# Kernel optimization log

Measured on AMD Instinct MI355X. Metric: run time of the kernel, lower is better.

The kernel has to match this reference:

```python
import jax, jax.numpy as jnp
import numpy as np
import math

N, E, D, R, L = 20000, 640000, 128, 16, 3
R_MAX = math.sqrt(2.0)
CENTERS = jnp.linspace(0.0, R_MAX, R)          # GaussianRBF centers on [0, sqrt(2)]
GAMMA = 1.0 / (2.0 * (R_MAX / (R - 1)) ** 2)   # 1/(2*sigma^2), sigma = center spacing


def _mlp(x, w1, b1, w2, b2):
    # mlp([din, d_h, dout]): Linear -> SiLU -> Linear (dropout=0.0)
    return jax.nn.silu(x @ w1 + b1) @ w2 + b2


def _ln(x, g, b):
    mu = jnp.mean(x, axis=-1, keepdims=True)
    v = jnp.var(x, axis=-1, keepdims=True)
    return (x - mu) * jax.lax.rsqrt(v + 1e-5) * g + b


def _time_emb(t):
    # SinusoidalEmbedding(dim=D)
    half = D // 2
    freqs = jnp.exp(-math.log(10000.0) * jnp.arange(half, dtype=jnp.float32) / (half - 1))
    a = t * freqs
    return jnp.concatenate([jnp.sin(a), jnp.cos(a)])


def setup_inputs():
    key = jax.random.key(0)
    ks = jax.random.split(key, 16)
    s = 0.05
    p = {}
    p["x_t"] = jax.random.normal(ks[0], (N, 3), dtype=jnp.float32)
    p["edge_index"] = jax.random.randint(ks[1], (2, E), 0, N)
    p["t"] = 25
    p["time_w1"] = jax.random.normal(ks[2], (D, D)) * s
    p["time_b1"] = jnp.zeros((D,))
    p["time_w2"] = jax.random.normal(ks[3], (D, D)) * s
    p["time_b2"] = jnp.zeros((D,))
    p["nodein_w1"] = jax.random.normal(ks[4], (3 + D, D)) * s
    p["nodein_b1"] = jnp.zeros((D,))
    p["nodein_w2"] = jax.random.normal(ks[5], (D, D)) * s
    p["nodein_b2"] = jnp.zeros((D,))
    p["phim_w1"] = jax.random.normal(ks[6], (L, 2 * D + R, D)) * s
    p["phim_b1"] = jnp.zeros((L, D))
    p["phim_w2"] = jax.random.normal(ks[7], (L, D, D)) * s
    p["phim_b2"] = jnp.zeros((L, D))
    p["phih_w1"] = jax.random.normal(ks[8], (L, 2 * D, D)) * s
    p["phih_b1"] = jnp.zeros((L, D))
    p["phih_w2"] = jax.random.normal(ks[9], (L, D, D)) * s
    p["phih_b2"] = jnp.zeros((L, D))
    p["ln_g"] = jnp.ones((L, D))
    p["ln_b"] = jnp.zeros((L, D))
    p["out_w1"] = jax.random.normal(ks[10], (D, D)) * s
    p["out_b1"] = jnp.zeros((D,))
    p["out_w2"] = jax.random.normal(ks[11], (D, 3)) * s
    p["out_b2"] = jnp.zeros((3,))
    return p


def reference(x_t, edge_index, t,
              time_w1, time_b1, time_w2, time_b2,
              nodein_w1, nodein_b1, nodein_w2, nodein_b2,
              phim_w1, phim_b1, phim_w2, phim_b2,
              phih_w1, phih_b1, phih_w2, phih_b2,
              ln_g, ln_b,
              out_w1, out_b1, out_w2, out_b2):
    # GraphDenoiser.forward: one denoiser call of the diffusion sampling loop.
    n = x_t.shape[0]
    src, dst = edge_index[0], edge_index[1]

    te = _mlp(_time_emb(jnp.asarray(t, jnp.float32)), time_w1, time_b1, time_w2, time_b2)
    h = _mlp(jnp.concatenate([x_t, jnp.broadcast_to(te, (n, D))], axis=-1),
             nodein_w1, nodein_b1, nodein_w2, nodein_b2)

    # edge geometry is fixed across layers (depends only on x_t)
    dx = x_t[src, :2] - x_t[dst, :2]                     # [E, 2]
    r = jnp.sqrt(jnp.sum(dx * dx, axis=-1) + 1e-8)       # [E]
    rbf = jnp.exp(-GAMMA * (r[:, None] - CENTERS) ** 2)  # [E, R]

    for i in range(L):  # WeightedInvariantMPNNLayer x L (edge_weight == 1)
        m_in = jnp.concatenate([h[src], h[dst], rbf], axis=-1)      # [E, 2D+R]
        m = _mlp(m_in, phim_w1[i], phim_b1[i], phim_w2[i], phim_b2[i])
        agg = jax.ops.segment_sum(m, dst, num_segments=n)           # scatter_sum
        h_up = _mlp(jnp.concatenate([h, agg], axis=-1),
                    phih_w1[i], phih_b1[i], phih_w2[i], phih_b2[i])
        h = _ln(h + h_up, ln_g[i], ln_b[i])

    return _mlp(h, out_w1, out_b1, out_w2, out_b2)  # predicted eps, [N, 3]
```

## Files before the change

kernel.cpp:

```cpp
#include <hip/hip_runtime.h>

typedef unsigned short u16;
typedef unsigned int u32;

#define NNODES 20000
#define NEDGES 640000
#define RBF_GAMMA 56.25f
#define SQRT2 1.4142135623730951f
#define PITCH 132
#define BPITCH 136

typedef __bf16 bf16x8 __attribute__((ext_vector_type(8)));
typedef __bf16 bf16x2 __attribute__((ext_vector_type(2)));
typedef float f32x4 __attribute__((ext_vector_type(4)));

__device__ __forceinline__ float b2f(u16 u) {
    union { float f; u32 i; } x; x.i = ((u32)u) << 16; return x.f;
}
__device__ __forceinline__ float hi2f(u32 w) {
    union { float f; u32 i; } x; x.i = w & 0xffff0000u; return x.f;
}
__device__ __forceinline__ float lo2f(u32 w) {
    union { float f; u32 i; } x; x.i = w << 16; return x.f;
}
__device__ __forceinline__ u16 f2b(float f) {
    union { float f; u32 i; } x; x.f = f;
    u32 r = (x.i + 0x7fffu + ((x.i >> 16) & 1u)) >> 16;
    return (u16)r;
}
__device__ __forceinline__ u32 pack2(float a, float b) {
#if __has_builtin(__builtin_amdgcn_cvt_pk_bf16_f32)
    union { bf16x2 v; u32 u; } x;
    x.v = __builtin_amdgcn_cvt_pk_bf16_f32(a, b);
    return x.u;
#else
    return (u32)f2b(a) | ((u32)f2b(b) << 16);
#endif
}
__device__ __forceinline__ float silu(float v) {
    return v * __builtin_amdgcn_rcpf(1.0f + __expf(-v));
}
__device__ __forceinline__ void fma4(float4 w, float4 s, float& acc) {
    acc = fmaf(w.x, s.x, acc);
    acc = fmaf(w.y, s.y, acc);
    acc = fmaf(w.z, s.z, acc);
    acc = fmaf(w.w, s.w, acc);
}

__global__ __launch_bounds__(256) void k_hist(const int* __restrict__ ei, int* __restrict__ hist) {
    int e = blockIdx.x * 256 + threadIdx.x;
    atomicAdd(&hist[ei[NEDGES + e]], 1);
}

__global__ __launch_bounds__(1024) void k_scan(const int* __restrict__ hist,
                                               int* __restrict__ row_ptr,
                                               int* __restrict__ cursor) {
    __shared__ int psum[1024];
    int t = threadIdx.x;
    int base = t * 20;
    int s = 0;
    if (base < NNODES)
        for (int i = 0; i < 20; ++i) s += hist[base + i];
    psum[t] = s;
    __syncthreads();
    for (int off = 1; off < 1024; off <<= 1) {
        int v = (t >= off) ? psum[t - off] : 0;
        __syncthreads();
        psum[t] += v;
        __syncthreads();
    }
    int excl = psum[t] - s;
    if (base < NNODES) {
        int run = excl;
        for (int i = 0; i < 20; ++i) {
            row_ptr[base + i] = run;
            cursor[base + i] = run;
            run += hist[base + i];
        }
    }
    if (t == 1023) row_ptr[NNODES] = psum[1023];
}

__global__ __launch_bounds__(256) void k_scatter(const int* __restrict__ ei, int* __restrict__ cursor,
                                                 int* __restrict__ ssrc, int* __restrict__ sdst) {
    int e = blockIdx.x * 256 + threadIdx.x;
    int d = ei[NEDGES + e];
    int pos = atomicAdd(&cursor[d], 1);
    ssrc[pos] = ei[e];
    sdst[pos] = d;
}

__global__ __launch_bounds__(256) void k_prep_wr(const float* __restrict__ pmw1,
                                                 const float* __restrict__ pmb1,
                                                 u16* __restrict__ Wr) {
    int id = blockIdx.x * 256 + threadIdx.x;
    if (id >= 1536) return;
    int l = id / 512; int r = id - l * 512;
    int nt = r >> 6, lane = r & 63;
    int col = nt * 16 + (lane & 15);
    alignas(16) u16 tmp[8];
    #pragma unroll
    for (int jj = 0; jj < 8; ++jj) {
        int kk = (lane >> 4) * 8 + jj;
        float v = 0.f;
        if (kk < 16) v = pmw1[l * 34816 + (256 + kk) * 128 + col];
        else if (kk == 16) v = pmb1[l * 128 + col];
        tmp[jj] = f2b(v);
    }
    *(uint4*)(Wr + (size_t)id * 8) = *(const uint4*)tmp;
}

struct BfM { const float* s[18]; };
__global__ __launch_bounds__(256) void k_prep_bf(BfM bf, u16* __restrict__ dst) {
    int id = blockIdx.x * 256 + threadIdx.x;
    if (id >= 36864) return;
    int mat = id >> 11;
    bool lomode = (mat >= 13 && mat != 16);
    int r = id & 2047;
    int kc = r >> 9;
    int r2 = r & 511;
    int nt = r2 >> 6, lane = r2 & 63;
    int col = nt * 16 + (lane & 15);
    int kb = kc * 32 + (lane >> 4) * 8;
    const float* src = bf.s[mat];
    alignas(16) u16 tmp[8];
    #pragma unroll
    for (int jj = 0; jj < 8; ++jj) {
        float v = src[(kb + jj) * 128 + col];
        u16 h = f2b(v);
        tmp[jj] = lomode ? f2b(v - b2f(h)) : h;
    }
    *(uint4*)(dst + (size_t)id * 8) = *(const uint4*)tmp;
}

__global__ __launch_bounds__(256) void k_prep_mbf(const float* __restrict__ Mp, u16* __restrict__ dst) {
    int id = blockIdx.x * 256 + threadIdx.x;
    if (id >= 12288) return;
    int mat = id >> 11;
    int l = mat >> 1, lomode = mat & 1;
    int r = id & 2047;
    int kc = r >> 9;
    int r2 = r & 511;
    int nt = r2 >> 6, lane = r2 & 63;
    int col = nt * 16 + (lane & 15);
    int kb = kc * 32 + (lane >> 4) * 8;
    const float* src = Mp + (size_t)l * 16384;
    alignas(16) u16 tmp[8];
    #pragma unroll
    for (int jj = 0; jj < 8; ++jj) {
        int k = kb + jj;
        float v = src[(k >> 2) * 512 + col * 4 + (k & 3)];
        u16 h = f2b(v);
        tmp[jj] = lomode ? f2b(v - b2f(h)) : h;
    }
    *(uint4*)(dst + (size_t)id * 8) = *(const uint4*)tmp;
}

struct PackM { const float* s[3]; float* d[3]; int K[3]; };
__global__ __launch_bounds__(256) void k_pack(PackM pm) {
    int m = blockIdx.y;
    int idx = blockIdx.x * 256 + threadIdx.x;
    if (idx >= pm.K[m] * 128) return;
    int k = idx >> 7, j = idx & 127;
    pm.d[m][(k >> 2) * 512 + j * 4 + (k & 3)] = pm.s[m][idx];
}

__global__ __launch_bounds__(256) void k_prep_m(const float* __restrict__ pmw2,
        const float* __restrict__ pmb2, const float* __restrict__ V1p,
        float* __restrict__ Mp, float* __restrict__ bvv) {
    const int l = blockIdx.y, bx = blockIdx.x;
    const float* V1 = V1p + (size_t)l * 32768;
    const int tid = threadIdx.x;
    const int w = tid >> 6, lane = tid & 63;
    const int cg = lane & 15, ng = lane >> 4;
    const int jc0 = w * 32 + cg * 2, jc1 = jc0 + 1;
    __shared__ alignas(16) float W2L[16][PITCH];
    __shared__ float b2L[128];
    if (bx < 8) {
        const float4* src = (const float4*)(pmw2 + (size_t)l * 16384 + bx * 16 * 128);
        for (int q = tid; q < 512; q += 256) {
            int row = q >> 5, part = q & 31;
            *(float4*)&W2L[row][part * 4] = src[q];
        }
        __syncthreads();
        int r0 = ng * 4;
        float acc[4][2];
        #pragma unroll
        for (int n = 0; n < 4; ++n) { acc[n][0] = 0.f; acc[n][1] = 0.f; }
        for (int mm = 0; mm < 32; ++mm) {
            float4 wa = *(const float4*)(V1 + (32 + mm) * 512 + jc0 * 4);
            float4 wb = *(const float4*)(V1 + (32 + mm) * 512 + jc1 * 4);
            #pragma unroll
            for (int n = 0; n < 4; ++n) {
                float4 s4 = *(const float4*)&W2L[r0 + n][mm * 4];
                fma4(wa, s4, acc[n][0]);
                fma4(wb, s4, acc[n][1]);
            }
        }
        #pragma unroll
        for (int n = 0; n < 4; ++n) {
            int kg = bx * 16 + r0 + n;
            Mp[(size_t)l * 16384 + (kg >> 2) * 512 + jc0 * 4 + (kg & 3)] = acc[n][0];
            Mp[(size_t)l * 16384 + (kg >> 2) * 512 + jc1 * 4 + (kg & 3)] = acc[n][1];
        }
    } else {
        if (tid < 128) b2L[tid] = pmb2[l * 128 + tid];
        __syncthreads();
        if (ng == 0) {
            float a0 = 0.f, a1 = 0.f;
            for (int mm = 0; mm < 32; ++mm) {
                float4 wa = *(const float4*)(V1 + (32 + mm) * 512 + jc0 * 4);
                float4 wb = *(const float4*)(V1 + (32 + mm) * 512 + jc1 * 4);
                float4 s4 = *(const float4*)&b2L[mm * 4];
                fma4(wa, s4, a0);
                fma4(wb, s4, a1);
            }
            bvv[l * 128 + jc0] = a0;
            bvv[l * 128 + jc1] = a1;
        }
    }
}

__global__ __launch_bounds__(128) void k_time(const int* __restrict__ tptr,
        const float* __restrict__ tw1, const float* __restrict__ tb1,
        const float* __restrict__ tw2, const float* __restrict__ tb2,
        const float* __restrict__ nw1, const float* __restrict__ nb1,
        float* __restrict__ base1) {
    __shared__ float emb[128], hid[128], te[128];
    int j = threadIdx.x;
    int raw = tptr[0];
    float tv;
    if (raw >= 0 && raw < (1 << 24)) tv = (float)raw;
    else tv = __int_as_float(raw);
    float fr = expf(-9.210340371976184f * (float)(j & 63) / 63.0f);
    float a = tv * fr;
    emb[j] = (j < 64) ? sinf(a) : cosf(a);
    __syncthreads();
    float acc = tb1[j];
    for (int k = 0; k < 128; ++k) acc += emb[k] * tw1[k * 128 + j];
    hid[j] = silu(acc);
    __syncthreads();
    acc = tb2[j];
    for (int k = 0; k < 128; ++k) acc += hid[k] * tw2[k * 128 + j];
    te[j] = acc;
    __syncthreads();
    acc = nb1[j];
    for (int k = 0; k < 128; ++k) acc += te[k] * nw1[(3 + k) * 128 + j];
    base1[j] = acc;
}

__global__ __launch_bounds__(256) void k_h0(const float* __restrict__ x, const float* __restrict__ base1,
        const float* __restrict__ nw1, const u16* __restrict__ nw2h, const u16* __restrict__ nw2l,
        const float* __restrict__ nb2, const u16* __restrict__ Yw,
        float* __restrict__ hf, u16* __restrict__ Ysrc, u16* __restrict__ Ydst) {
    const int tid = threadIdx.x;
    const int w = tid >> 6, lane = tid & 63;
    const int cg = lane & 15, ng = lane >> 4;
    const int jc0 = w * 32 + cg * 2, jc1 = jc0 + 1;
    const int n0 = ng * 4;
    const int base = blockIdx.x * 16;
    const int lrow = lane & 15, quad = lane >> 4;
    __shared__ alignas(16) float xl[16][4];
    __shared__ alignas(16) u16 hih[16 * BPITCH], hil[16 * BPITCH];
    __shared__ alignas(16) u16 hb16[16 * BPITCH];
    if (tid < 48) { int n = tid / 3, cc = tid - n * 3; xl[n][cc] = x[(size_t)(base + n) * 3 + cc]; }
    __syncthreads();
    {
        float w0a = nw1[jc0], w0b = nw1[jc1];
        float w1a = nw1[128 + jc0], w1b = nw1[128 + jc1];
        float w2a = nw1[256 + jc0], w2b = nw1[256 + jc1];
        float ba = base1[jc0], bb = base1[jc1];
        #pragma unroll
        for (int n = 0; n < 4; ++n) {
            int row = n0 + n;
            float x0 = xl[row][0], x1 = xl[row][1], x2 = xl[row][2];
            float va = silu(ba + x0 * w0a + x1 * w1a + x2 * w2a);
            float vb = silu(bb + x0 * w0b + x1 * w1b + x2 * w2b);
            u32 hw = pack2(va, vb);
            *(u32*)&hih[row * BPITCH + jc0] = hw;
            *(u32*)&hil[row * BPITCH + jc0] = pack2(va - lo2f(hw), vb - hi2f(hw));
        }
    }
    __syncthreads();
    {
        bf16x8 ah[4], al[4];
        #pragma unroll
        for (int kc = 0; kc < 4; ++kc) {
            ah[kc] = *(const bf16x8*)(hih + lrow * BPITCH + kc * 32 + quad * 8);
            al[kc] = *(const bf16x8*)(hil + lrow * BPITCH + kc * 32 + quad * 8);
        }
        #pragma unroll
        for (int t = 0; t < 2; ++t) {
            int nt = w * 2 + t;
            f32x4 a4 = {0.f, 0.f, 0.f, 0.f};
            #pragma unroll
            for (int kc = 0; kc < 4; ++kc) {
                size_t o = (size_t)((kc * 8 + nt) * 512 + lane * 8);
                bf16x8 bh = *(const bf16x8*)(nw2h + o);
                bf16x8 bl = *(const bf16x8*)(nw2l + o);
                a4 = __builtin_amdgcn_mfma_f32_16x16x32_bf16(ah[kc], bh, a4, 0, 0, 0);
                a4 = __builtin_amdgcn_mfma_f32_16x16x32_bf16(al[kc], bh, a4, 0, 0, 0);
                a4 = __builtin_amdgcn_mfma_f32_16x16x32_bf16(ah[kc], bl, a4, 0, 0, 0);
            }
            int colC = nt * 16 + lrow;
            float bC = nb2[colC];
            #pragma unroll
            for (int r = 0; r < 4; ++r) {
                int R = quad * 4 + r;
                float v = a4[r] + bC;
                hf[(size_t)(base + R) * 128 + colC] = v;
                hb16[R * BPITCH + colC] = f2b(v);
            }
        }
    }
    __syncthreads();
    {
        const int mat = w >> 1, half = w & 1;
        bf16x8 a[4];
        #pragma unroll
        for (int kc = 0; kc < 4; ++kc)
            a[kc] = *(const bf16x8*)(hb16 + lrow * BPITCH + kc * 32 + quad * 8);
        u16* dst = mat ? Ydst : Ysrc;
        #pragma unroll
        for (int t = 0; t < 4; ++t) {
            int nt = half * 4 + t;
            f32x4 a4 = {0.f, 0.f, 0.f, 0.f};
            #pragma unroll
            for (int kc = 0; kc < 4; ++kc) {
                bf16x8 b = *(const bf16x8*)(Yw + (size_t)(((mat * 4 + kc) * 8 + nt) * 512 + lane * 8));
                a4 = __builtin_amdgcn_mfma_f32_16x16x32_bf16(a[kc], b, a4, 0, 0, 0);
            }
            #pragma unroll
            for (int r = 0; r < 4; ++r)
                dst[(size_t)(base + quad * 4 + r) * 128 + nt * 16 + lrow] = f2b(a4[r]);
        }
    }
}

__global__ __launch_bounds__(512, 8) void k_edge(
        const u16* __restrict__ Ysrc, const u16* __restrict__ Ydst,
        const float* __restrict__ x,
        const int* __restrict__ ssrc, const int* __restrict__ sdst,
        const u16* __restrict__ Wr,
        float* __restrict__ s_glob) {
    __shared__ alignas(16) u16 sst[128 * 72];
    __shared__ alignas(16) u16 ys[64 * 128];
    __shared__ float rv[64];
    __shared__ int s_d[65];
    __shared__ int s_s[64];
    const int tid = threadIdx.x;
    const int e0 = blockIdx.x * 64;
    if (tid < 64) {
        int s = ssrc[e0 + tid], d = sdst[e0 + tid];
        s_s[tid] = s; s_d[tid] = d;
        float ddx = x[s * 3] - x[d * 3];
        float ddy = x[s * 3 + 1] - x[d * 3 + 1];
        rv[tid] = sqrtf(ddx * ddx + ddy * ddy + 1e-8f);
    } else if (tid == 64) {
        s_d[64] = -1;
    }
    __syncthreads();
    #pragma unroll
    for (int i = 0; i < 2; ++i) {
        int cch = tid + i * 512;
        int e = cch >> 4, part = cch & 15;
        *(uint4*)(ys + e * 128 + part * 8) = *(const uint4*)(Ysrc + (size_t)s_s[e] * 128 + part * 8);
    }
    const int w = tid >> 6, lane = tid & 63;
    const int m = w & 3, nh = w >> 2;
    const int lrow = lane & 15, quad = lane >> 4;
    float r = rv[m * 16 + lrow];
    union { bf16x8 v; u16 u[8]; } af;
    #pragma unroll
    for (int j = 0; j < 8; ++j) {
        int kk = quad * 8 + j;
        float v;
        if (kk < 16) {
            float dd = r - SQRT2 * (float)kk / 15.0f;
            v = __expf(-RBF_GAMMA * dd * dd);
        } else v = (kk == 16) ? 1.0f : 0.0f;
        af.u[j] = f2b(v);
    }
    {
        const u16* Bp = Wr + lane * 8;
        #pragma unroll
        for (int t = 0; t < 4; ++t) {
            int nt = nh * 4 + t;
            f32x4 a4 = {0.f, 0.f, 0.f, 0.f};
            bf16x8 b = *(const bf16x8*)(Bp + nt * 512);
            a4 = __builtin_amdgcn_mfma_f32_16x16x32_bf16(af.v, b, a4, 0, 0, 0);
            int col = nt * 16 + lrow;
            u32 lo = pack2(a4[0], a4[1]);
            u32 hi = pack2(a4[2], a4[3]);
            *(uint2*)(sst + col * 72 + m * 16 + quad * 4) = make_uint2(lo, hi);
        }
    }
    __syncthreads();
    {
        const int col = tid & 127, q = tid >> 7;
        const int r0 = q * 16;
        float a = 0.f;
        int cd = s_d[r0];
        float yd = b2f(Ydst[(size_t)cd * 128 + col]);
        #pragma unroll
        for (int h = 0; h < 2; ++h) {
            uint4 c0 = *(const uint4*)(sst + col * 72 + r0 + h * 8);
            float sv8[8];
            sv8[0] = lo2f(c0.x); sv8[1] = hi2f(c0.x);
            sv8[2] = lo2f(c0.y); sv8[3] = hi2f(c0.y);
            sv8[4] = lo2f(c0.z); sv8[5] = hi2f(c0.z);
            sv8[6] = lo2f(c0.w); sv8[7] = hi2f(c0.w);
            #pragma unroll
            for (int i = 0; i < 8; ++i) {
                int rr = r0 + h * 8 + i;
                int nd = s_d[rr + 1];
                float v = sv8[i] + b2f(ys[rr * 128 + col]) + yd;
                a += silu(v);
                bool last = (h == 1 && i == 7);
                if (last || nd != cd) {
                    atomicAdd(&s_glob[(size_t)cd * 128 + col], a);
                    a = 0.f;
                    if (!last && nd != cd)
                        yd = b2f(Ydst[(size_t)nd * 128 + col]);
                }
                cd = nd;
            }
        }
    }
}

__global__ __launch_bounds__(256) void k_node(float* __restrict__ s_glob, const int* __restrict__ row_ptr,
        float* __restrict__ hf,
        const u16* __restrict__ V1h, const u16* __restrict__ V1l,
        const u16* __restrict__ Mh, const u16* __restrict__ Ml,
        const u16* __restrict__ V2bf,
        const float* __restrict__ bv, const float* __restrict__ c1, const float* __restrict__ c2,
        const float* __restrict__ lng, const float* __restrict__ lnb,
        const u16* __restrict__ Yw,
        u16* __restrict__ Ysrc, u16* __restrict__ Ydst,
        const u16* __restrict__ ow1bf, const float* __restrict__ ob1,
        const float* __restrict__ ow2, const float* __restrict__ ob2,
        float* __restrict__ out) {
    const int tid = threadIdx.x;
    const int w = tid >> 6, lane = tid & 63;
    const int cg = lane & 15, ng = lane >> 4;
    const int jc0 = w * 32 + cg * 2, jc1 = jc0 + 1;
    const int n0 = ng * 4;
    const int base = blockIdx.x * 16;
    const int lrow = lane & 15, quad = lane >> 4;
    __shared__ alignas(16) float hv[16][PITCH];
    __shared__ alignas(16) float xs[16][PITCH];
    __shared__ alignas(16) u16 hvh[16 * BPITCH], hvl[16 * BPITCH];
    __shared__ alignas(16) u16 svh[16 * BPITCH], svl[16 * BPITCH];
    __shared__ alignas(16) u16 ybf[16 * BPITCH];
    __shared__ float mv[16][2];
    __shared__ int rp[17];

    if (tid < 17) rp[tid] = row_ptr[base + tid];
    {
        const float4* sg4 = (const float4*)(s_glob + (size_t)base * 128);
        float4* sg4w = (float4*)(s_glob + (size_t)base * 128);
        const float4* hg4 = (const float4*)(hf + (size_t)base * 128);
        for (int q = tid; q < 512; q += 256) {
            int row = q >> 5, part = q & 31;
            float4 s = sg4[q];
            float4 h = hg4[q];
            if (Yw != nullptr) sg4w[q] = make_float4(0.f, 0.f, 0.f, 0.f);
            *(float4*)&hv[row][part * 4] = h;
            u32 hw0 = pack2(h.x, h.y), hw1 = pack2(h.z, h.w);
            *(uint2*)&hvh[row * BPITCH + part * 4] = make_uint2(hw0, hw1);
            u32 hl0 = pack2(h.x - lo2f(hw0), h.y - hi2f(hw0));
            u32 hl1 = pack2(h.z - lo2f(hw1), h.w - hi2f(hw1));
            *(uint2*)&hvl[row * BPITCH + part * 4] = make_uint2(hl0, hl1);
            u32 sw0 = pack2(s.x, s.y), sw1 = pack2(s.z, s.w);
            *(uint2*)&svh[row * BPITCH + part * 4] = make_uint2(sw0, sw1);
            u32 sl0 = pack2(s.x - lo2f(sw0), s.y - hi2f(sw0));
            u32 sl1 = pack2(s.z - lo2f(sw1), s.w - hi2f(sw1));
            *(uint2*)&svl[row * BPITCH + part * 4] = make_uint2(sl0, sl1);
        }
    }
    __syncthreads();

    {
        bf16x8 ahh[4], ahl[4], ash[4], asl[4];
        #pragma unroll
        for (int kc = 0; kc < 4; ++kc) {
            ahh[kc] = *(const bf16x8*)(hvh + lrow * BPITCH + kc * 32 + quad * 8);
            ahl[kc] = *(const bf16x8*)(hvl + lrow * BPITCH + kc * 32 + quad * 8);
            ash[kc] = *(const bf16x8*)(svh + lrow * BPITCH + kc * 32 + quad * 8);
            asl[kc] = *(const bf16x8*)(svl + lrow * BPITCH + kc * 32 + quad * 8);
        }
        float dg[4];
        #pragma unroll
        for (int r = 0; r < 4; ++r)
            dg[r] = (float)(rp[quad * 4 + r + 1] - rp[quad * 4 + r]);
        #pragma unroll
        for (int t = 0; t < 2; ++t) {
            int nt = w * 2 + t;
            f32x4 a4 = {0.f, 0.f, 0.f, 0.f};
            #pragma unroll
            for (int kc = 0; kc < 4; ++kc) {
                size_t o = (size_t)((kc * 8 + nt) * 512 + lane * 8);
                bf16x8 bh = *(const bf16x8*)(V1h + o);
                bf16x8 bl = *(const bf16x8*)(V1l + o);
                a4 = __builtin_amdgcn_mfma_f32_16x16x32_bf16(ahh[kc], bh, a4, 0, 0, 0);
                a4 = __builtin_amdgcn_mfma_f32_16x16x32_bf16(ahl[kc], bh, a4, 0, 0, 0);
                a4 = __builtin_amdgcn_mfma_f32_16x16x32_bf16(ahh[kc], bl, a4, 0, 0, 0);
                bf16x8 mh = *(const bf16x8*)(Mh + o);
                bf16x8 ml = *(const bf16x8*)(Ml + o);
                a4 = __builtin_amdgcn_mfma_f32_16x16x32_bf16(ash[kc], mh, a4, 0, 0, 0);
                a4 = __builtin_amdgcn_mfma_f32_16x16x32_bf16(asl[kc], mh, a4, 0, 0, 0);
                a4 = __builtin_amdgcn_mfma_f32_16x16x32_bf16(ash[kc], ml, a4, 0, 0, 0);
            }
            int colC = nt * 16 + lrow;
            float bvC = bv[colC], c1C = c1[colC];
            #pragma unroll
            for (int r = 0; r < 4; ++r) {
                float u = a4[r] + dg[r] * bvC + c1C;
                ybf[(quad * 4 + r) * BPITCH + colC] = f2b(silu(u));
            }
        }
    }
    __syncthreads();
    {
        bf16x8 a[4];
        #pragma unroll
        for (int kc = 0; kc < 4; ++kc)
            a[kc] = *(const bf16x8*)(ybf + lrow * BPITCH + kc * 32 + quad * 8);
        #pragma unroll
        for (int t = 0; t < 2; ++t) {
            int nt = w * 2 + t;
            f32x4 a4 = {0.f, 0.f, 0.f, 0.f};
            #pragma unroll
            for (int kc = 0; kc < 4; ++kc) {
                bf16x8 b = *(const bf16x8*)(V2bf + (size_t)((kc * 8 + nt) * 512 + lane * 8));
                a4 = __builtin_amdgcn_mfma_f32_16x16x32_bf16(a[kc], b, a4, 0, 0, 0);
            }
            int colC = nt * 16 + lrow;
            float c2v = c2[colC];
            #pragma unroll
            for (int r = 0; r < 4; ++r) {
                int R = quad * 4 + r;
                xs[R][colC] = a4[r] + c2v + hv[R][colC];
            }
        }
    }
    __syncthreads();
    {
        int row = tid >> 4, part = tid & 15;
        float4 a = *(const float4*)&xs[row][part * 8];
        float4 b = *(const float4*)&xs[row][part * 8 + 4];
        float s1 = a.x + a.y + a.z + a.w + b.x + b.y + b.z + b.w;
        float s2 = a.x * a.x + a.y * a.y + a.z * a.z + a.w * a.w
                 + b.x * b.x + b.y * b.y + b.z * b.z + b.w * b.w;
        #pragma unroll
        for (int mq = 1; mq < 16; mq <<= 1) {
            s1 += __shfl_xor(s1, mq, 64);
            s2 += __shfl_xor(s2, mq, 64);
        }
        if (part == 0) { mv[row][0] = s1; mv[row][1] = s2; }
    }
    __syncthreads();
    {
        float ga = lng[jc0], gb = lng[jc1];
        float bba = lnb[jc0], bbb = lnb[jc1];
        #pragma unroll
        for (int n = 0; n < 4; ++n) {
            int row = n0 + n;
            float mu = mv[row][0] * (1.0f / 128.0f);
            float var = mv[row][1] * (1.0f / 128.0f) - mu * mu;
            float rs = rsqrtf(var + 1e-5f);
            float y0 = (xs[row][jc0] - mu) * rs * ga + bba;
            float y1 = (xs[row][jc1] - mu) * rs * gb + bbb;
            if (Yw != nullptr)
                *(float2*)&hf[(size_t)(base + row) * 128 + jc0] = make_float2(y0, y1);
            *(u32*)&ybf[row * BPITCH + jc0] = pack2(y0, y1);
        }
    }
    if (Yw != nullptr) {
        __syncthreads();
        const int mat = w >> 1, half = w & 1;
        bf16x8 a[4];
        #pragma unroll
        for (int kc = 0; kc < 4; ++kc)
            a[kc] = *(const bf16x8*)(ybf + lrow * BPITCH + kc * 32 + quad * 8);
        u16* dst = mat ? Ydst : Ysrc;
        #pragma unroll
        for (int t = 0; t < 4; ++t) {
            int nt = half * 4 + t;
            f32x4 a4 = {0.f, 0.f, 0.f, 0.f};
            #pragma unroll
            for (int kc = 0; kc < 4; ++kc) {
                bf16x8 b = *(const bf16x8*)(Yw + (size_t)(((mat * 4 + kc) * 8 + nt) * 512 + lane * 8));
                a4 = __builtin_amdgcn_mfma_f32_16x16x32_bf16(a[kc], b, a4, 0, 0, 0);
            }
            #pragma unroll
            for (int r = 0; r < 4; ++r)
                dst[(size_t)(base + quad * 4 + r) * 128 + nt * 16 + lrow] = f2b(a4[r]);
        }
    } else {
        __syncthreads();
        {
            bf16x8 a[4];
            #pragma unroll
            for (int kc = 0; kc < 4; ++kc)
                a[kc] = *(const bf16x8*)(ybf + lrow * BPITCH + kc * 32 + quad * 8);
            #pragma unroll
            for (int t = 0; t < 2; ++t) {
                int nt = w * 2 + t;
                f32x4 a4 = {0.f, 0.f, 0.f, 0.f};
                #pragma unroll
                for (int kc = 0; kc < 4; ++kc) {
                    bf16x8 b = *(const bf16x8*)(ow1bf + (size_t)((kc * 8 + nt) * 512 + lane * 8));
                    a4 = __builtin_amdgcn_mfma_f32_16x16x32_bf16(a[kc], b, a4, 0, 0, 0);
                }
                int colC = nt * 16 + lrow;
                float b1v = ob1[colC];
                #pragma unroll
                for (int r = 0; r < 4; ++r)
                    hv[quad * 4 + r][colC] = silu(a4[r] + b1v);
            }
        }
        __syncthreads();
        {
            int row = tid >> 4, s = tid & 15;
            float p0 = 0.f, p1 = 0.f, p2 = 0.f;
            #pragma unroll
            for (int kk2 = 0; kk2 < 8; ++kk2) {
                int k = s * 8 + kk2;
                float h2 = hv[row][k];
                p0 = fmaf(h2, ow2[k * 3 + 0], p0);
                p1 = fmaf(h2, ow2[k * 3 + 1], p1);
                p2 = fmaf(h2, ow2[k * 3 + 2], p2);
            }
            #pragma unroll
            for (int mq = 1; mq < 16; mq <<= 1) {
                p0 += __shfl_xor(p0, mq, 64);
                p1 += __shfl_xor(p1, mq, 64);
                p2 += __shfl_xor(p2, mq, 64);
            }
            if (s == 0) {
                float* o = out + (size_t)(base + row) * 3;
                o[0] = p0 + ob2[0];
                o[1] = p1 + ob2[1];
                o[2] = p2 + ob2[2];
            }
        }
    }
}

extern "C" void kernel_launch(void* const* d_in, const int* in_sizes, int n_in,
                              void* d_out, int out_size, void* d_ws, size_t ws_size,
                              hipStream_t stream) {
    const float* x    = (const float*)d_in[0];
    const int* ei     = (const int*)d_in[1];
    const int* tptr   = (const int*)d_in[2];
    const float* tw1  = (const float*)d_in[3];
    const float* tb1  = (const float*)d_in[4];
    const float* tw2  = (const float*)d_in[5];
    const float* tb2  = (const float*)d_in[6];
    const float* nw1  = (const float*)d_in[7];
    const float* nb1  = (const float*)d_in[8];
    const float* nw2  = (const float*)d_in[9];
    const float* nb2  = (const float*)d_in[10];
    const float* pmw1 = (const float*)d_in[11];
    const float* pmb1 = (const float*)d_in[12];
    const float* pmw2 = (const float*)d_in[13];
    const float* pmb2 = (const float*)d_in[14];
    const float* phw1 = (const float*)d_in[15];
    const float* phb1 = (const float*)d_in[16];
    const float* phw2 = (const float*)d_in[17];
    const float* phb2 = (const float*)d_in[18];
    const float* lng  = (const float*)d_in[19];
    const float* lnb  = (const float*)d_in[20];
    const float* ow1  = (const float*)d_in[21];
    const float* ob1  = (const float*)d_in[22];
    const float* ow2  = (const float*)d_in[23];
    const float* ob2  = (const float*)d_in[24];
    float* out = (float*)d_out;

    char* wsp = (char*)d_ws;
    size_t off = 0;
    auto alloc = [&](size_t bytes) -> void* {
        void* p = wsp + off;
        off += (bytes + 255) & ~(size_t)255;
        return p;
    };
    int* hist    = (int*)alloc((size_t)NNODES * 4);
    int* cursor  = (int*)alloc((size_t)NNODES * 4);
    int* row_ptr = (int*)alloc((size_t)(NNODES + 1) * 4);
    int* ssrc    = (int*)alloc((size_t)NEDGES * 4);
    int* sdst    = (int*)alloc((size_t)NEDGES * 4);
    u16* Wr      = (u16*)alloc((size_t)3 * 8 * 64 * 8 * 2);
    u16* BF      = (u16*)alloc((size_t)18 * 16384 * 2);
    u16* Mf      = (u16*)alloc((size_t)6 * 16384 * 2);
    float* base1 = (float*)alloc(128 * 4);
    float* V1p   = (float*)alloc((size_t)3 * 256 * 128 * 4);
    float* Mp    = (float*)alloc((size_t)3 * 128 * 128 * 4);
    float* bvv   = (float*)alloc((size_t)3 * 128 * 4);
    float* hf    = (float*)alloc((size_t)NNODES * 128 * 4);
    u16* Ysrc    = (u16*)alloc((size_t)NNODES * 128 * 2);
    u16* Ydst    = (u16*)alloc((size_t)NNODES * 128 * 2);
    float* s_glob= (float*)alloc((size_t)NNODES * 128 * 4);

    (void)hipMemsetAsync(hist, 0, (size_t)NNODES * 4, stream);
    k_hist<<<NEDGES / 256, 256, 0, stream>>>(ei, hist);
    k_scan<<<1, 1024, 0, stream>>>(hist, row_ptr, cursor);
    k_scatter<<<NEDGES / 256, 256, 0, stream>>>(ei, cursor, ssrc, sdst);
    k_prep_wr<<<6, 256, 0, stream>>>(pmw1, pmb1, Wr);

    BfM bf;
    for (int l = 0; l < 3; ++l) {
        bf.s[l * 2 + 0] = pmw1 + (size_t)l * 34816;
        bf.s[l * 2 + 1] = pmw1 + (size_t)l * 34816 + 16384;
        bf.s[6 + l] = phw2 + (size_t)l * 16384;
        bf.s[10 + l] = phw1 + (size_t)l * 32768;
        bf.s[13 + l] = phw1 + (size_t)l * 32768;
    }
    bf.s[9] = ow1;
    bf.s[16] = nw2;
    bf.s[17] = nw2;
    k_prep_bf<<<144, 256, 0, stream>>>(bf, BF);

    PackM pm;
    for (int l = 0; l < 3; ++l) {
        pm.s[l] = phw1 + (size_t)l * 32768; pm.d[l] = V1p + (size_t)l * 32768; pm.K[l] = 256;
    }
    k_pack<<<dim3(128, 3), 256, 0, stream>>>(pm);
    k_prep_m<<<dim3(9, 3), 256, 0, stream>>>(pmw2, pmb2, V1p, Mp, bvv);
    k_prep_mbf<<<48, 256, 0, stream>>>(Mp, Mf);

    k_time<<<1, 128, 0, stream>>>(tptr, tw1, tb1, tw2, tb2, nw1, nb1, base1);
    k_h0<<<1250, 256, 0, stream>>>(x, base1, nw1,
            BF + (size_t)16 * 16384, BF + (size_t)17 * 16384, nb2, BF, hf, Ysrc, Ydst);

    (void)hipMemsetAsync(s_glob, 0, (size_t)NNODES * 128 * 4, stream);
    for (int l = 0; l < 3; ++l) {
        k_edge<<<NEDGES / 64, 512, 0, stream>>>(Ysrc, Ydst, x, ssrc, sdst,
                Wr + (size_t)l * 4096, s_glob);
        const u16* YwN = (l < 2) ? (BF + (size_t)(l + 1) * 32768) : nullptr;
        k_node<<<1250, 256, 0, stream>>>(s_glob, row_ptr, hf,
                BF + (size_t)(10 + l) * 16384, BF + (size_t)(13 + l) * 16384,
                Mf + (size_t)(l * 2) * 16384, Mf + (size_t)(l * 2 + 1) * 16384,
                BF + (size_t)(6 + l) * 16384,
                bvv + l * 128, phb1 + l * 128, phb2 + l * 128, lng + l * 128, lnb + l * 128,
                YwN, Ysrc, Ydst,
                BF + (size_t)9 * 16384, ob1, ow2, ob2, out);
    }
}
```

Before: 505.3 us.

## Compute source-side message projection per edge instead of precomputing per node

Previously each node's h was projected through the src half of phi_m's first layer (Ysrc), and edges gathered that projection. Now nodes store bf16 h, and each edge block gathers h[src] into shared memory and runs an extra K=128 MFMA per output tile, with the src weights fused alongside the RBF/bias weights. This drops one node-level GEMM and one N×128 projection buffer, but moves the projection to 640k edges instead of 20k nodes, adding about 32x more MFMA work in the edge kernel plus extra shared memory and a sync.

```diff
diff --git a/kernel.cpp b/kernel.cpp
--- a/kernel.cpp
+++ b/kernel.cpp
@@ -90,32 +90,39 @@
     sdst[pos] = d;
 }
 
-__global__ __launch_bounds__(256) void k_prep_wr(const float* __restrict__ pmw1,
+__global__ __launch_bounds__(256) void k_prep_w5(const float* __restrict__ pmw1,
                                                  const float* __restrict__ pmb1,
-                                                 u16* __restrict__ Wr) {
+                                                 u16* __restrict__ Wf) {
     int id = blockIdx.x * 256 + threadIdx.x;
-    if (id >= 1536) return;
-    int l = id / 512; int r = id - l * 512;
-    int nt = r >> 6, lane = r & 63;
+    if (id >= 7680) return;
+    int l = id / 2560; int r = id - l * 2560;
+    int kc = r >> 9;
+    int r2 = r & 511;
+    int nt = r2 >> 6, lane = r2 & 63;
     int col = nt * 16 + (lane & 15);
     alignas(16) u16 tmp[8];
     #pragma unroll
     for (int jj = 0; jj < 8; ++jj) {
-        int kk = (lane >> 4) * 8 + jj;
-        float v = 0.f;
-        if (kk < 16) v = pmw1[l * 34816 + (256 + kk) * 128 + col];
-        else if (kk == 16) v = pmb1[l * 128 + col];
+        int kl = (lane >> 4) * 8 + jj;
+        float v;
+        if (kc < 4) {
+            v = pmw1[l * 34816 + (kc * 32 + kl) * 128 + col];
+        } else {
+            if (kl < 16) v = pmw1[l * 34816 + (256 + kl) * 128 + col];
+            else if (kl == 16) v = pmb1[l * 128 + col];
+            else v = 0.f;
+        }
         tmp[jj] = f2b(v);
     }
-    *(uint4*)(Wr + (size_t)id * 8) = *(const uint4*)tmp;
-}
-
-struct BfM { const float* s[18]; };
+    *(uint4*)(Wf + (size_t)id * 8) = *(const uint4*)tmp;
+}
+
+struct BfM { const float* s[15]; };
 __global__ __launch_bounds__(256) void k_prep_bf(BfM bf, u16* __restrict__ dst) {
     int id = blockIdx.x * 256 + threadIdx.x;
-    if (id >= 36864) return;
+    if (id >= 30720) return;
     int mat = id >> 11;
-    bool lomode = (mat >= 13 && mat != 16);
+    bool lomode = (mat >= 10 && mat != 13);
     int r = id & 2047;
     int kc = r >> 9;
     int r2 = r & 511;
@@ -252,7 +259,7 @@
 __global__ __launch_bounds__(256) void k_h0(const float* __restrict__ x, const float* __restrict__ base1,
         const float* __restrict__ nw1, const u16* __restrict__ nw2h, const u16* __restrict__ nw2l,
         const float* __restrict__ nb2, const u16* __restrict__ Yw,
-        float* __restrict__ hf, u16* __restrict__ Ysrc, u16* __restrict__ Ydst) {
+        float* __restrict__ hf, u16* __restrict__ hbf, u16* __restrict__ Ydst) {
     const int tid = threadIdx.x;
     const int w = tid >> 6, lane = tid & 63;
     const int cg = lane & 15, ng = lane >> 4;
@@ -315,36 +322,39 @@
     }
     __syncthreads();
     {
-        const int mat = w >> 1, half = w & 1;
         bf16x8 a[4];
         #pragma unroll
         for (int kc = 0; kc < 4; ++kc)
             a[kc] = *(const bf16x8*)(hb16 + lrow * BPITCH + kc * 32 + quad * 8);
-        u16* dst = mat ? Ydst : Ysrc;
-        #pragma unroll
-        for (int t = 0; t < 4; ++t) {
-            int nt = half * 4 + t;
+        #pragma unroll
+        for (int t = 0; t < 2; ++t) {
+            int nt = w * 2 + t;
             f32x4 a4 = {0.f, 0.f, 0.f, 0.f};
             #pragma unroll
             for (int kc = 0; kc < 4; ++kc) {
-                bf16x8 b = *(const bf16x8*)(Yw + (size_t)(((mat * 4 + kc) * 8 + nt) * 512 + lane * 8));
+                bf16x8 b = *(const bf16x8*)(Yw + (size_t)((kc * 8 + nt) * 512 + lane * 8));
                 a4 = __builtin_amdgcn_mfma_f32_16x16x32_bf16(a[kc], b, a4, 0, 0, 0);
             }
             #pragma unroll
             for (int r = 0; r < 4; ++r)
-                dst[(size_t)(base + quad * 4 + r) * 128 + nt * 16 + lrow] = f2b(a4[r]);
+                Ydst[(size_t)(base + quad * 4 + r) * 128 + nt * 16 + lrow] = f2b(a4[r]);
+        }
+        for (int q = tid; q < 512; q += 256) {
+            int row = q >> 5, part = q & 31;
+            *(uint2*)&hbf[(size_t)(base + row) * 128 + part * 4] =
+                *(const uint2*)&hb16[row * BPITCH + part * 4];
         }
     }
 }
 
 __global__ __launch_bounds__(512, 8) void k_edge(
-        const u16* __restrict__ Ysrc, const u16* __restrict__ Ydst,
+        const u16* __restrict__ hbf, const u16* __restrict__ Ydst,
         const float* __restrict__ x,
         const int* __restrict__ ssrc, const int* __restrict__ sdst,
-        const u16* __restrict__ Wr,
+        const u16* __restrict__ Wf,
         float* __restrict__ s_glob) {
     __shared__ alignas(16) u16 sst[128 * 72];
-    __shared__ alignas(16) u16 ys[64 * 128];
+    __shared__ alignas(16) u16 hs[64 * BPITCH];
     __shared__ float rv[64];
     __shared__ int s_d[65];
     __shared__ int s_s[64];
@@ -364,7 +374,7 @@
     for (int i = 0; i < 2; ++i) {
         int cch = tid + i * 512;
         int e = cch >> 4, part = cch & 15;
-        *(uint4*)(ys + e * 128 + part * 8) = *(const uint4*)(Ysrc + (size_t)s_s[e] * 128 + part * 8);
+        *(uint4*)(hs + e * BPITCH + part * 8) = *(const uint4*)(hbf + (size_t)s_s[e] * 128 + part * 8);
     }
     const int w = tid >> 6, lane = tid & 63;
     const int m = w & 3, nh = w >> 2;
@@ -381,14 +391,25 @@
         } else v = (kk == 16) ? 1.0f : 0.0f;
         af.u[j] = f2b(v);
     }
-    {
-        const u16* Bp = Wr + lane * 8;
+    __syncthreads();
+    {
+        bf16x8 a[4];
+        #pragma unroll
+        for (int kc = 0; kc < 4; ++kc)
+            a[kc] = *(const bf16x8*)(hs + (m * 16 + lrow) * BPITCH + kc * 32 + quad * 8);
         #pragma unroll
         for (int t = 0; t < 4; ++t) {
             int nt = nh * 4 + t;
             f32x4 a4 = {0.f, 0.f, 0.f, 0.f};
-            bf16x8 b = *(const bf16x8*)(Bp + nt * 512);
-            a4 = __builtin_amdgcn_mfma_f32_16x16x32_bf16(af.v, b, a4, 0, 0, 0);
+            #pragma unroll
+            for (int kc = 0; kc < 4; ++kc) {
+                bf16x8 b = *(const bf16x8*)(Wf + (size_t)((kc * 8 + nt) * 512 + lane * 8));
+                a4 = __builtin_amdgcn_mfma_f32_16x16x32_bf16(a[kc], b, a4, 0, 0, 0);
+            }
+            {
+                bf16x8 b = *(const bf16x8*)(Wf + (size_t)((4 * 8 + nt) * 512 + lane * 8));
+                a4 = __builtin_amdgcn_mfma_f32_16x16x32_bf16(af.v, b, a4, 0, 0, 0);
+            }
             int col = nt * 16 + lrow;
             u32 lo = pack2(a4[0], a4[1]);
             u32 hi = pack2(a4[2], a4[3]);
@@ -414,7 +435,7 @@
             for (int i = 0; i < 8; ++i) {
                 int rr = r0 + h * 8 + i;
                 int nd = s_d[rr + 1];
-                float v = sv8[i] + b2f(ys[rr * 128 + col]) + yd;
+                float v = sv8[i] + yd;
                 a += silu(v);
                 bool last = (h == 1 && i == 7);
                 if (last || nd != cd) {
@@ -437,7 +458,7 @@
         const float* __restrict__ bv, const float* __restrict__ c1, const float* __restrict__ c2,
         const float* __restrict__ lng, const float* __restrict__ lnb,
         const u16* __restrict__ Yw,
-        u16* __restrict__ Ysrc, u16* __restrict__ Ydst,
+        u16* __restrict__ hbf, u16* __restrict__ Ydst,
         const u16* __restrict__ ow1bf, const float* __restrict__ ob1,
         const float* __restrict__ ow2, const float* __restrict__ ob2,
         float* __restrict__ out) {
@@ -579,24 +600,27 @@
     }
     if (Yw != nullptr) {
         __syncthreads();
-        const int mat = w >> 1, half = w & 1;
         bf16x8 a[4];
         #pragma unroll
         for (int kc = 0; kc < 4; ++kc)
             a[kc] = *(const bf16x8*)(ybf + lrow * BPITCH + kc * 32 + quad * 8);
-        u16* dst = mat ? Ydst : Ysrc;
-        #pragma unroll
-        for (int t = 0; t < 4; ++t) {
-            int nt = half * 4 + t;
+        #pragma unroll
+        for (int t = 0; t < 2; ++t) {
+            int nt = w * 2 + t;
             f32x4 a4 = {0.f, 0.f, 0.f, 0.f};
             #pragma unroll
             for (int kc = 0; kc < 4; ++kc) {
-                bf16x8 b = *(const bf16x8*)(Yw + (size_t)(((mat * 4 + kc) * 8 + nt) * 512 + lane * 8));
+                bf16x8 b = *(const bf16x8*)(Yw + (size_t)((kc * 8 + nt) * 512 + lane * 8));
                 a4 = __builtin_amdgcn_mfma_f32_16x16x32_bf16(a[kc], b, a4, 0, 0, 0);
             }
             #pragma unroll
             for (int r = 0; r < 4; ++r)
-                dst[(size_t)(base + quad * 4 + r) * 128 + nt * 16 + lrow] = f2b(a4[r]);
+                Ydst[(size_t)(base + quad * 4 + r) * 128 + nt * 16 + lrow] = f2b(a4[r]);
+        }
+        for (int q = tid; q < 512; q += 256) {
+            int row = q >> 5, part = q & 31;
+            *(uint2*)&hbf[(size_t)(base + row) * 128 + part * 4] =
+                *(const uint2*)&ybf[row * BPITCH + part * 4];
         }
     } else {
         __syncthreads();
@@ -691,15 +715,15 @@
     int* row_ptr = (int*)alloc((size_t)(NNODES + 1) * 4);
     int* ssrc    = (int*)alloc((size_t)NEDGES * 4);
     int* sdst    = (int*)alloc((size_t)NEDGES * 4);
-    u16* Wr      = (u16*)alloc((size_t)3 * 8 * 64 * 8 * 2);
-    u16* BF      = (u16*)alloc((size_t)18 * 16384 * 2);
+    u16* Wf      = (u16*)alloc((size_t)3 * 20480 * 2);
+    u16* BF      = (u16*)alloc((size_t)15 * 16384 * 2);
     u16* Mf      = (u16*)alloc((size_t)6 * 16384 * 2);
     float* base1 = (float*)alloc(128 * 4);
     float* V1p   = (float*)alloc((size_t)3 * 256 * 128 * 4);
     float* Mp    = (float*)alloc((size_t)3 * 128 * 128 * 4);
     float* bvv   = (float*)alloc((size_t)3 * 128 * 4);
     float* hf    = (float*)alloc((size_t)NNODES * 128 * 4);
-    u16* Ysrc    = (u16*)alloc((size_t)NNODES * 128 * 2);
+    u16* hbf     = (u16*)alloc((size_t)NNODES * 128 * 2);
     u16* Ydst    = (u16*)alloc((size_t)NNODES * 128 * 2);
     float* s_glob= (float*)alloc((size_t)NNODES * 128 * 4);
 
@@ -707,20 +731,19 @@
     k_hist<<<NEDGES / 256, 256, 0, stream>>>(ei, hist);
     k_scan<<<1, 1024, 0, stream>>>(hist, row_ptr, cursor);
     k_scatter<<<NEDGES / 256, 256, 0, stream>>>(ei, cursor, ssrc, sdst);
-    k_prep_wr<<<6, 256, 0, stream>>>(pmw1, pmb1, Wr);
+    k_prep_w5<<<30, 256, 0, stream>>>(pmw1, pmb1, Wf);
 
     BfM bf;
     for (int l = 0; l < 3; ++l) {
-        bf.s[l * 2 + 0] = pmw1 + (size_t)l * 34816;
-        bf.s[l * 2 + 1] = pmw1 + (size_t)l * 34816 + 16384;
-        bf.s[6 + l] = phw2 + (size_t)l * 16384;
+        bf.s[l]     = pmw1 + (size_t)l * 34816 + 16384;
+        bf.s[3 + l] = phw2 + (size_t)l * 16384;
+        bf.s[7 + l] = phw1 + (size_t)l * 32768;
         bf.s[10 + l] = phw1 + (size_t)l * 32768;
-        bf.s[13 + l] = phw1 + (size_t)l * 32768;
-    }
-    bf.s[9] = ow1;
-    bf.s[16] = nw2;
-    bf.s[17] = nw2;
-    k_prep_bf<<<144, 256, 0, stream>>>(bf, BF);
+    }
+    bf.s[6] = ow1;
+    bf.s[13] = nw2;
+    bf.s[14] = nw2;
+    k_prep_bf<<<120, 256, 0, stream>>>(bf, BF);
 
     PackM pm;
     for (int l = 0; l < 3; ++l) {
@@ -732,19 +755,20 @@
 
     k_time<<<1, 128, 0, stream>>>(tptr, tw1, tb1, tw2, tb2, nw1, nb1, base1);
     k_h0<<<1250, 256, 0, stream>>>(x, base1, nw1,
-            BF + (size_t)16 * 16384, BF + (size_t)17 * 16384, nb2, BF, hf, Ysrc, Ydst);
+            BF + (size_t)13 * 16384, BF + (size_t)14 * 16384, nb2,
+            BF , hf, hbf, Ydst);
 
     (void)hipMemsetAsync(s_glob, 0, (size_t)NNODES * 128 * 4, stream);
     for (int l = 0; l < 3; ++l) {
-        k_edge<<<NEDGES / 64, 512, 0, stream>>>(Ysrc, Ydst, x, ssrc, sdst,
-                Wr + (size_t)l * 4096, s_glob);
-        const u16* YwN = (l < 2) ? (BF + (size_t)(l + 1) * 32768) : nullptr;
+        k_edge<<<NEDGES / 64, 512, 0, stream>>>(hbf, Ydst, x, ssrc, sdst,
+                Wf + (size_t)l * 20480, s_glob);
+        const u16* YwN = (l < 2) ? (BF + (size_t)(l + 1) * 16384) : nullptr;
         k_node<<<1250, 256, 0, stream>>>(s_glob, row_ptr, hf,
-                BF + (size_t)(10 + l) * 16384, BF + (size_t)(13 + l) * 16384,
+                BF + (size_t)(7 + l) * 16384, BF + (size_t)(10 + l) * 16384,
                 Mf + (size_t)(l * 2) * 16384, Mf + (size_t)(l * 2 + 1) * 16384,
-                BF + (size_t)(6 + l) * 16384,
+                BF + (size_t)(3 + l) * 16384,
                 bvv + l * 128, phb1 + l * 128, phb2 + l * 128, lng + l * 128, lnb + l * 128,
-                YwN, Ysrc, Ydst,
-                BF + (size_t)9 * 16384, ob1, ow2, ob2, out);
-    }
-}
+                YwN, hbf, Ydst,
+                BF + (size_t)6 * 16384, ob1, ow2, ob2, out);
+    }
+}
```

After: 555.4 us. 1.1x slower.
